# Performance work log

Hardware: AMD Instinct MI355X
Metric: run time of the kernel (lower is better)

The kernel has to match this reference:

```python
import jax, jax.numpy as jnp
import numpy as np

N_CH = 8      # n_channel (complex symbols)
L = 3         # channel taps
R = 0.5       # code rate k/n = 4/8
EBNO_DB = 7.0
EPS = 1e-5    # BatchNorm eps
NOISE_SCALE = float(1.0 / np.sqrt(2.0 * R * (10.0 ** (EBNO_DB / 10.0))))


def conv1d(x, w, b, stride=1):
    # x: [B, Cin, W], w: [Cout, Cin, K]
    y = jax.lax.conv_general_dilated(x, w, (stride,), 'VALID',
                                     dimension_numbers=('NCH', 'OIH', 'NCH'))
    return y + b[None, :, None]


def setup_inputs() -> dict:
    key = jax.random.key(0)
    ks = jax.random.split(key, 24)
    B = 262144
    s = 0.1  # weight scale for numerical stability
    inp = {
        'x': jax.random.normal(ks[0], (B, 16), jnp.float32),
        'noise': jax.random.normal(ks[1], (B, 16), jnp.float32),
        'fading': jax.random.normal(ks[2], (B, L, 2), jnp.float32) / np.sqrt(2.0),
        'ew1': jax.random.normal(ks[3], (16, 16), jnp.float32) * s,
        'eb1': jnp.zeros((16,), jnp.float32),
        'ew2': jax.random.normal(ks[4], (16, 16), jnp.float32) * s,
        'eb2': jnp.zeros((16,), jnp.float32),
        'bng': jnp.ones((16,), jnp.float32),
        'bnb': jnp.zeros((16,), jnp.float32),
        'pc1w': jax.random.normal(ks[5], (16, 1, 4), jnp.float32) * s,
        'pc1b': jnp.zeros((16,), jnp.float32),
        'pc2w': jax.random.normal(ks[6], (16, 16, 2), jnp.float32) * s,
        'pc2b': jnp.zeros((16,), jnp.float32),
        'pc3w': jax.random.normal(ks[7], (16, 16, 2), jnp.float32) * s,
        'pc3b': jnp.zeros((16,), jnp.float32),
        'pc4w': jax.random.normal(ks[8], (16, 16, 1), jnp.float32) * s,
        'pc4b': jnp.zeros((16,), jnp.float32),
        'pc5w': jax.random.normal(ks[9], (16, 16, 3), jnp.float32) * s,
        'pc5b': jnp.zeros((16,), jnp.float32),
        'plw': jax.random.normal(ks[10], (16, 16), jnp.float32) * s,
        'plb': jnp.ones((16,), jnp.float32),  # keep h estimate away from 0 (complex division)
        'dc1w': jax.random.normal(ks[11], (8, 1, 1), jnp.float32) * s,
        'dc1b': jnp.zeros((8,), jnp.float32),
        'dc2w': jax.random.normal(ks[12], (8, 8, 2), jnp.float32) * s,
        'dc2b': jnp.zeros((8,), jnp.float32),
        'dc3w': jax.random.normal(ks[13], (8, 8, 1), jnp.float32) * s,
        'dc3b': jnp.zeros((8,), jnp.float32),
        'dc4w': jax.random.normal(ks[14], (8, 8, 1), jnp.float32) * s,
        'dc4b': jnp.zeros((8,), jnp.float32),
        'dl1w': jax.random.normal(ks[15], (16, 64), jnp.float32) * s,
        'dl1b': jnp.zeros((16,), jnp.float32),
        'dl2w': jax.random.normal(ks[16], (16, 16), jnp.float32) * s,
        'dl2b': jnp.zeros((16,), jnp.float32),
        'dl3w': jax.random.normal(ks[17], (16, 16), jnp.float32) * s,
        'dl3b': jnp.zeros((16,), jnp.float32),
    }
    return inp


def reference(x, noise, fading, ew1, eb1, ew2, eb2, bng, bnb,
              pc1w, pc1b, pc2w, pc2b, pc3w, pc3b, pc4w, pc4b, pc5w, pc5b,
              plw, plb, dc1w, dc1b, dc2w, dc2b, dc3w, dc3b, dc4w, dc4b,
              dl1w, dl1b, dl2w, dl2b, dl3w, dl3b):
    B = x.shape[0]
    # ---- encoder: Linear -> ELU -> Linear -> BatchNorm1d (batch stats) ----
    h1 = jax.nn.elu(x @ ew1.T + eb1)
    z = h1 @ ew2.T + eb2
    mu = z.mean(0)
    var = ((z - mu) ** 2).mean(0)
    z = (z - mu) / jnp.sqrt(var + EPS) * bng + bnb
    # ---- rayleigh channel: complex FIR over L taps (vectorized) ----
    zc = z.reshape(B, N_CH, 2)
    c = jax.lax.complex(zc[..., 0], zc[..., 1])            # [B, 8] complex
    hf = jax.lax.complex(fading[..., 0], fading[..., 1])   # [B, 3] complex
    padded = jnp.pad(c, ((0, 0), (2, 2)))                  # [B, 12]
    idx = jnp.arange(N_CH + L - 1)[:, None] + jnp.arange(L)[None, :]  # [10, 3]
    win = padded[:, idx]                                   # [B, 10, 3]
    out = jnp.einsum('bij,bj->bi', win, hf[:, ::-1])[:, :N_CH]
    creal = jnp.stack([out.real, out.imag], -1).reshape(B, 2 * N_CH) + noise * NOISE_SCALE
    # ---- parameter estimation (conv stack) ----
    p = creal[:, None, :]                                  # [B, 1, 16]
    p = jax.nn.relu(conv1d(p, pc1w, pc1b, 1))              # [B,16,13]
    p = jax.nn.relu(conv1d(p, pc2w, pc2b, 1))              # [B,16,12]
    p = jax.nn.relu(conv1d(p, pc3w, pc3b, 4))              # [B,16,3]
    p = jax.nn.relu(conv1d(p, pc4w, pc4b, 1))              # [B,16,3]
    p = jax.nn.relu(conv1d(p, pc5w, pc5b, 1))              # [B,16,1]
    hhat = p.reshape(B, -1) @ plw.T + plb                  # [B,16]
    # ---- transform: complex equalization c / h ----
    cc2 = creal.reshape(B, N_CH, 2)
    hh2 = hhat.reshape(B, N_CH, 2)
    cc = jax.lax.complex(cc2[..., 0], cc2[..., 1])
    hh = jax.lax.complex(hh2[..., 0], hh2[..., 1])
    t = cc / hh
    treal = jnp.stack([t.real, t.imag], -1).reshape(B, 2 * N_CH)
    # ---- decoder (conv stack + MLP; dropout omitted / eval mode) ----
    d = treal[:, None, :]
    d = jax.nn.relu(conv1d(d, dc1w, dc1b, 1))              # [B,8,16]
    d = jax.nn.relu(conv1d(d, dc2w, dc2b, 2))              # [B,8,8]
    d = jax.nn.relu(conv1d(d, dc3w, dc3b, 1))
    d = jax.nn.relu(conv1d(d, dc4w, dc4b, 1))
    d = d.reshape(B, -1)                                   # [B,64]
    d = jax.nn.relu(d @ dl1w.T + dl1b)
    d = jax.nn.elu(d @ dl2w.T + dl2b)
    return d @ dl3w.T + dl3b
```

## Files before the change

kernel.cpp:

```cpp
#include <hip/hip_runtime.h>
#include <math.h>

#define NSCALE 0.44668359215096315f

typedef float v2f __attribute__((ext_vector_type(2)));

__device__ __forceinline__ v2f fma2(v2f a, v2f b, v2f c) { return __builtin_elementwise_fma(a, b, c); }
__device__ __forceinline__ float eluf(float v)  { return v > 0.0f ? v : __expf(v) - 1.0f; }
__device__ __forceinline__ float reluf(float v) { return fmaxf(v, 0.0f); }

__device__ __forceinline__ float dot16p(const float* __restrict__ w, const v2f p[8], float b) {
    const v2f* w2 = reinterpret_cast<const v2f*>(w);
    v2f a = {b, 0.0f};
#pragma unroll
    for (int q = 0; q < 8; ++q) a = fma2(w2[q], p[q], a);
    return a.x + a.y;
}
__device__ __forceinline__ float dot32p(const float* __restrict__ w, const v2f p[16], float b) {
    const v2f* w2 = reinterpret_cast<const v2f*>(w);
    v2f a = {b, 0.0f};
#pragma unroll
    for (int q = 0; q < 16; ++q) a = fma2(w2[q], p[q], a);
    return a.x + a.y;
}
__device__ __forceinline__ float dot8p(const float* __restrict__ w, const v2f p[4], float b) {
    const v2f* w2 = reinterpret_cast<const v2f*>(w);
    v2f a = {b, 0.0f};
#pragma unroll
    for (int q = 0; q < 4; ++q) a = fma2(w2[q], p[q], a);
    return a.x + a.y;
}

__global__ __launch_bounds__(256) void kW(const float* __restrict__ pc2w,
                                          const float* __restrict__ pc5w,
                                          const float* __restrict__ dl1w,
                                          float* __restrict__ pc2s,
                                          float* __restrict__ pc5s,
                                          float* __restrict__ dl1s)
{
    int tid = threadIdx.x;
    for (int j = tid; j < 512; j += 256) {
        int o = j >> 5, r = j & 31, ci = r >> 1, tap = r & 1;
        pc2s[tap*256 + o*16 + ci] = pc2w[j];
    }
    for (int j = tid; j < 768; j += 256) {
        int o = j / 48, r = j - o*48, ci = r / 3, g = r - ci*3;
        pc5s[g*256 + o*16 + ci] = pc5w[j];
    }
    for (int j = tid; j < 1024; j += 256) {
        int o = j >> 6, r = j & 63, c = r >> 3, t = r & 7;
        dl1s[t*128 + o*8 + c] = dl1w[j];
    }
}

__global__ __launch_bounds__(256) void kA(const float* __restrict__ x,
                                          const float* __restrict__ ew1, const float* __restrict__ eb1,
                                          const float* __restrict__ ew2, const float* __restrict__ eb2,
                                          float* __restrict__ partials, float* __restrict__ zout, int B)
{
    __shared__ float wsum[4][32];
    int tid = threadIdx.x;
    int i = blockIdx.x * 256 + tid;
    bool valid = i < B;
    v2f x2[8];
    if (valid) {
        const float4* xp = reinterpret_cast<const float4*>(x + (size_t)i * 16);
#pragma unroll
        for (int q = 0; q < 4; ++q) {
            float4 v = xp[q];
            x2[2*q+0] = {v.x, v.y};
            x2[2*q+1] = {v.z, v.w};
        }
    } else {
#pragma unroll
        for (int q = 0; q < 8; ++q) x2[q] = {0.0f, 0.0f};
    }

    v2f h1p[8];
#pragma unroll
    for (int j = 0; j < 8; ++j) {
        float r0 = eluf(dot16p(ew1 + (2*j+0)*16, x2, eb1[2*j+0]));
        float r1 = eluf(dot16p(ew1 + (2*j+1)*16, x2, eb1[2*j+1]));
        h1p[j] = {r0, r1};
    }
    float z[16];
#pragma unroll
    for (int o = 0; o < 16; ++o) {
        float a = dot16p(ew2 + o*16, h1p, eb2[o]);
        z[o] = valid ? a : 0.0f;
    }

    if (valid) {
        float4* zp = reinterpret_cast<float4*>(zout + (size_t)i * 16);
        zp[0] = make_float4(z[0],  z[1],  z[2],  z[3]);
        zp[1] = make_float4(z[4],  z[5],  z[6],  z[7]);
        zp[2] = make_float4(z[8],  z[9],  z[10], z[11]);
        zp[3] = make_float4(z[12], z[13], z[14], z[15]);
    }

    int lane = tid & 63, wave = tid >> 6;
#pragma unroll
    for (int c = 0; c < 16; ++c) {
        float s = z[c];
        float q = z[c] * z[c];
#pragma unroll
        for (int m = 1; m < 64; m <<= 1) { s += __shfl_xor(s, m); q += __shfl_xor(q, m); }
        if (lane == 0) { wsum[wave][c] = s; wsum[wave][16 + c] = q; }
    }
    __syncthreads();
    if (tid < 32) {
        float t = wsum[0][tid] + wsum[1][tid] + wsum[2][tid] + wsum[3][tid];
        partials[(size_t)blockIdx.x * 32 + tid] = t;
    }
}

__global__ __launch_bounds__(256) void kB(const float* __restrict__ partials, int nblk, int B,
                                          const float* __restrict__ bng, const float* __restrict__ bnb,
                                          float* __restrict__ bnp)
{
    int tid = threadIdx.x;
    int q = tid >> 3, k = tid & 7;
    int chunk = (nblk + 7) / 8;
    int j0 = k * chunk;
    int j1 = j0 + chunk; if (j1 > nblk) j1 = nblk;
    double s = 0.0;
    for (int j = j0; j < j1; ++j) s += (double)partials[(size_t)j * 32 + q];
    s += __shfl_xor(s, 4);
    s += __shfl_xor(s, 2);
    s += __shfl_xor(s, 1);
    __shared__ double tot[32];
    if (k == 0) tot[q] = s;
    __syncthreads();
    if (tid < 16) {
        double mu  = tot[tid] / (double)B;
        double var = tot[16 + tid] / (double)B - mu * mu;
        double a = (double)bng[tid] / sqrt(var + 1e-5);
        double b = (double)bnb[tid] - mu * a;
        bnp[tid]      = (float)a;
        bnp[16 + tid] = (float)b;
    }
}

__global__ __launch_bounds__(256) void k23(float* __restrict__ crt,
    const float* __restrict__ fading, const float* __restrict__ noise,
    const float* __restrict__ bnp,
    const float* __restrict__ pc1w, const float* __restrict__ pc1b,
    const float* __restrict__ pc2s, const float* __restrict__ pc2b,
    const float* __restrict__ pc3w, const float* __restrict__ pc3b,
    const float* __restrict__ pc4w, const float* __restrict__ pc4b,
    const float* __restrict__ pc5s, const float* __restrict__ pc5b,
    const float* __restrict__ plw,  const float* __restrict__ plb,
    int B)
{
    int i = blockIdx.x * 256 + threadIdx.x;
    if (i >= B) return;

    {
        float zn[16];
        const float4* zp = reinterpret_cast<const float4*>(crt + (size_t)i * 16);
#pragma unroll
        for (int q = 0; q < 4; ++q) {
            float4 v = zp[q];
            zn[4*q+0] = fmaf(v.x, bnp[4*q+0], bnp[16 + 4*q+0]);
            zn[4*q+1] = fmaf(v.y, bnp[4*q+1], bnp[16 + 4*q+1]);
            zn[4*q+2] = fmaf(v.z, bnp[4*q+2], bnp[16 + 4*q+2]);
            zn[4*q+3] = fmaf(v.w, bnp[4*q+3], bnp[16 + 4*q+3]);
        }
        float f[6];
        const float2* fp = reinterpret_cast<const float2*>(fading + (size_t)i * 6);
#pragma unroll
        for (int q = 0; q < 3; ++q) { float2 v = fp[q]; f[2*q] = v.x; f[2*q+1] = v.y; }
        float cr[16];
#pragma unroll
        for (int n = 0; n < 8; ++n) {
            float re = f[0]*zn[2*n]   - f[1]*zn[2*n+1];
            float im = f[0]*zn[2*n+1] + f[1]*zn[2*n];
            if (n >= 1) { re += f[2]*zn[2*n-2] - f[3]*zn[2*n-1];
                          im += f[2]*zn[2*n-1] + f[3]*zn[2*n-2]; }
            if (n >= 2) { re += f[4]*zn[2*n-4] - f[5]*zn[2*n-3];
                          im += f[4]*zn[2*n-3] + f[5]*zn[2*n-4]; }
            cr[2*n] = re; cr[2*n+1] = im;
        }
        const float4* np_ = reinterpret_cast<const float4*>(noise + (size_t)i * 16);
#pragma unroll
        for (int q = 0; q < 4; ++q) {
            float4 v = np_[q];
            cr[4*q+0] = fmaf(v.x, NSCALE, cr[4*q+0]);
            cr[4*q+1] = fmaf(v.y, NSCALE, cr[4*q+1]);
            cr[4*q+2] = fmaf(v.z, NSCALE, cr[4*q+2]);
            cr[4*q+3] = fmaf(v.w, NSCALE, cr[4*q+3]);
        }
        float4* op = reinterpret_cast<float4*>(crt + (size_t)i * 16);
        op[0] = make_float4(cr[0],  cr[1],  cr[2],  cr[3]);
        op[1] = make_float4(cr[4],  cr[5],  cr[6],  cr[7]);
        op[2] = make_float4(cr[8],  cr[9],  cr[10], cr[11]);
        op[3] = make_float4(cr[12], cr[13], cr[14], cr[15]);
    }

    v2f p5acc[16];
#pragma unroll
    for (int o = 0; o < 16; ++o) p5acc[o] = {pc5b[o], 0.0f};

#pragma unroll 1
    for (int g = 0; g < 3; ++g) {
        float crg[8];
        {
            const float4* cp = reinterpret_cast<const float4*>(crt + (size_t)i * 16 + 4 * g);
            float4 v0 = cp[0], v1 = cp[1];
            crg[0]=v0.x; crg[1]=v0.y; crg[2]=v0.z; crg[3]=v0.w;
            crg[4]=v1.x; crg[5]=v1.y; crg[6]=v1.z; crg[7]=v1.w;
        }
        v2f p1p[3][8];
#pragma unroll
        for (int c2 = 0; c2 < 3; ++c2) {
#pragma unroll
            for (int j = 0; j < 8; ++j) {
                float4 w0 = *reinterpret_cast<const float4*>(pc1w + (2*j+0)*4);
                float4 w1 = *reinterpret_cast<const float4*>(pc1w + (2*j+1)*4);
                float a0 = pc1b[2*j+0], a1 = pc1b[2*j+1];
                a0 = fmaf(w0.x, crg[c2+0], a0); a0 = fmaf(w0.y, crg[c2+1], a0);
                a0 = fmaf(w0.z, crg[c2+2], a0); a0 = fmaf(w0.w, crg[c2+3], a0);
                a1 = fmaf(w1.x, crg[c2+0], a1); a1 = fmaf(w1.y, crg[c2+1], a1);
                a1 = fmaf(w1.z, crg[c2+2], a1); a1 = fmaf(w1.w, crg[c2+3], a1);
                p1p[c2][j] = {reluf(a0), reluf(a1)};
            }
        }
        v2f p2pair[16];
#pragma unroll
        for (int o = 0; o < 16; ++o) {
            const v2f* w0 = reinterpret_cast<const v2f*>(pc2s + o*16);
            const v2f* w1 = reinterpret_cast<const v2f*>(pc2s + 256 + o*16);
            v2f a0 = {pc2b[o], 0.0f}, a1 = {pc2b[o], 0.0f};
#pragma unroll
            for (int q = 0; q < 8; ++q) {
                v2f v0 = w0[q], v1 = w1[q];
                a0 = fma2(v0, p1p[0][q], a0);
                a0 = fma2(v1, p1p[1][q], a0);
                a1 = fma2(v0, p1p[1][q], a1);
                a1 = fma2(v1, p1p[2][q], a1);
            }
            p2pair[o] = {reluf(a0.x + a0.y), reluf(a1.x + a1.y)};
        }
        v2f p3p[8];
#pragma unroll
        for (int j = 0; j < 8; ++j) {
            float r0 = reluf(dot32p(pc3w + (2*j+0)*32, p2pair, pc3b[2*j+0]));
            float r1 = reluf(dot32p(pc3w + (2*j+1)*32, p2pair, pc3b[2*j+1]));
            p3p[j] = {r0, r1};
        }
        v2f p4p[8];
#pragma unroll
        for (int j = 0; j < 8; ++j) {
            float r0 = reluf(dot16p(pc4w + (2*j+0)*16, p3p, pc4b[2*j+0]));
            float r1 = reluf(dot16p(pc4w + (2*j+1)*16, p3p, pc4b[2*j+1]));
            p4p[j] = {r0, r1};
        }
#pragma unroll
        for (int o = 0; o < 16; ++o) {
            const v2f* w = reinterpret_cast<const v2f*>(pc5s + g*256 + o*16);
            v2f a = p5acc[o];
#pragma unroll
            for (int q = 0; q < 8; ++q) a = fma2(w[q], p4p[q], a);
            p5acc[o] = a;
        }
    }

    v2f p5p[8];
#pragma unroll
    for (int j = 0; j < 8; ++j) {
        float r0 = reluf(p5acc[2*j+0].x + p5acc[2*j+0].y);
        float r1 = reluf(p5acc[2*j+1].x + p5acc[2*j+1].y);
        p5p[j] = {r0, r1};
    }
    float hh[16];
#pragma unroll
    for (int o = 0; o < 16; ++o) hh[o] = dot16p(plw + o*16, p5p, plb[o]);

    float cr[16];
    {
        const float4* cp = reinterpret_cast<const float4*>(crt + (size_t)i * 16);
#pragma unroll
        for (int q = 0; q < 4; ++q) {
            float4 v = cp[q];
            cr[4*q+0] = v.x; cr[4*q+1] = v.y; cr[4*q+2] = v.z; cr[4*q+3] = v.w;
        }
    }
    float tr[16];
#pragma unroll
    for (int n = 0; n < 8; ++n) {
        float a = cr[2*n], b = cr[2*n+1];
        float c = hh[2*n], d = hh[2*n+1];
        float inv = 1.0f / (c*c + d*d);
        tr[2*n]   = (a*c + b*d) * inv;
        tr[2*n+1] = (b*c - a*d) * inv;
    }
    float4* op = reinterpret_cast<float4*>(crt + (size_t)i * 16);
    op[0] = make_float4(tr[0],  tr[1],  tr[2],  tr[3]);
    op[1] = make_float4(tr[4],  tr[5],  tr[6],  tr[7]);
    op[2] = make_float4(tr[8],  tr[9],  tr[10], tr[11]);
    op[3] = make_float4(tr[12], tr[13], tr[14], tr[15]);
}

__global__ __launch_bounds__(256) void k4(const float* __restrict__ trt,
    const float* __restrict__ dc1w, const float* __restrict__ dc1b,
    const float* __restrict__ dc2w, const float* __restrict__ dc2b,
    const float* __restrict__ dc3w, const float* __restrict__ dc3b,
    const float* __restrict__ dc4w, const float* __restrict__ dc4b,
    const float* __restrict__ dl1s, const float* __restrict__ dl1b,
    const float* __restrict__ dl2w, const float* __restrict__ dl2b,
    const float* __restrict__ dl3w, const float* __restrict__ dl3b,
    float* __restrict__ out, int B)
{
    int i = blockIdx.x * 256 + threadIdx.x;
    if (i >= B) return;

    v2f y2[16];
#pragma unroll
    for (int o = 0; o < 16; ++o) y2[o] = {dl1b[o], 0.0f};

#pragma unroll 1
    for (int t = 0; t < 8; ++t) {
        float2 tv = *reinterpret_cast<const float2*>(trt + (size_t)i * 16 + 2 * t);
        v2f d1p[8];
#pragma unroll
        for (int c = 0; c < 8; ++c) {
            float w = dc1w[c], b = dc1b[c];
            d1p[c] = {reluf(fmaf(w, tv.x, b)), reluf(fmaf(w, tv.y, b))};
        }
        v2f d2p[4];
#pragma unroll
        for (int j = 0; j < 4; ++j) {
            float r0 = reluf(dot16p(dc2w + (2*j+0)*16, d1p, dc2b[2*j+0]));
            float r1 = reluf(dot16p(dc2w + (2*j+1)*16, d1p, dc2b[2*j+1]));
            d2p[j] = {r0, r1};
        }
        v2f d3p[4];
#pragma unroll
        for (int j = 0; j < 4; ++j) {
            float r0 = reluf(dot8p(dc3w + (2*j+0)*8, d2p, dc3b[2*j+0]));
            float r1 = reluf(dot8p(dc3w + (2*j+1)*8, d2p, dc3b[2*j+1]));
            d3p[j] = {r0, r1};
        }
        v2f d4p[4];
#pragma unroll
        for (int j = 0; j < 4; ++j) {
            float r0 = reluf(dot8p(dc4w + (2*j+0)*8, d3p, dc4b[2*j+0]));
            float r1 = reluf(dot8p(dc4w + (2*j+1)*8, d3p, dc4b[2*j+1]));
            d4p[j] = {r0, r1};
        }
#pragma unroll
        for (int o = 0; o < 16; ++o) {
            const v2f* w = reinterpret_cast<const v2f*>(dl1s + t*128 + o*8);
            v2f a = y2[o];
#pragma unroll
            for (int q = 0; q < 4; ++q) a = fma2(w[q], d4p[q], a);
            y2[o] = a;
        }
    }

    v2f yp[8];
#pragma unroll
    for (int j = 0; j < 8; ++j) {
        float r0 = reluf(y2[2*j+0].x + y2[2*j+0].y);
        float r1 = reluf(y2[2*j+1].x + y2[2*j+1].y);
        yp[j] = {r0, r1};
    }
    v2f h2p[8];
#pragma unroll
    for (int j = 0; j < 8; ++j) {
        float r0 = eluf(dot16p(dl2w + (2*j+0)*16, yp, dl2b[2*j+0]));
        float r1 = eluf(dot16p(dl2w + (2*j+1)*16, yp, dl2b[2*j+1]));
        h2p[j] = {r0, r1};
    }
    float o16[16];
#pragma unroll
    for (int o = 0; o < 16; ++o) o16[o] = dot16p(dl3w + o*16, h2p, dl3b[o]);

    float4* op = reinterpret_cast<float4*>(out + (size_t)i * 16);
    op[0] = make_float4(o16[0],  o16[1],  o16[2],  o16[3]);
    op[1] = make_float4(o16[4],  o16[5],  o16[6],  o16[7]);
    op[2] = make_float4(o16[8],  o16[9],  o16[10], o16[11]);
    op[3] = make_float4(o16[12], o16[13], o16[14], o16[15]);
}

extern "C" void kernel_launch(void* const* d_in, const int* in_sizes, int n_in,
                              void* d_out, int out_size, void* d_ws, size_t ws_size,
                              hipStream_t stream)
{
    const float* x      = (const float*)d_in[0];
    const float* noise  = (const float*)d_in[1];
    const float* fading = (const float*)d_in[2];
    const float* ew1  = (const float*)d_in[3];
    const float* eb1  = (const float*)d_in[4];
    const float* ew2  = (const float*)d_in[5];
    const float* eb2  = (const float*)d_in[6];
    const float* bng  = (const float*)d_in[7];
    const float* bnb  = (const float*)d_in[8];
    const float* pc1w = (const float*)d_in[9];
    const float* pc1b = (const float*)d_in[10];
    const float* pc2w = (const float*)d_in[11];
    const float* pc2b = (const float*)d_in[12];
    const float* pc3w = (const float*)d_in[13];
    const float* pc3b = (const float*)d_in[14];
    const float* pc4w = (const float*)d_in[15];
    const float* pc4b = (const float*)d_in[16];
    const float* pc5w = (const float*)d_in[17];
    const float* pc5b = (const float*)d_in[18];
    const float* plw  = (const float*)d_in[19];
    const float* plb  = (const float*)d_in[20];
    const float* dc1w = (const float*)d_in[21];
    const float* dc1b = (const float*)d_in[22];
    const float* dc2w = (const float*)d_in[23];
    const float* dc2b = (const float*)d_in[24];
    const float* dc3w = (const float*)d_in[25];
    const float* dc3b = (const float*)d_in[26];
    const float* dc4w = (const float*)d_in[27];
    const float* dc4b = (const float*)d_in[28];
    const float* dl1w = (const float*)d_in[29];
    const float* dl1b = (const float*)d_in[30];
    const float* dl2w = (const float*)d_in[31];
    const float* dl2b = (const float*)d_in[32];
    const float* dl3w = (const float*)d_in[33];
    const float* dl3b = (const float*)d_in[34];

    int B = in_sizes[0] / 16;
    int nblk = (B + 255) / 256;

    float* partials = (float*)d_ws;
    float* bnp  = partials + (size_t)nblk * 32;
    float* pc2s = bnp + 32;
    float* pc5s = pc2s + 512;
    float* dl1s = pc5s + 768;
    float* crt  = dl1s + 1024;

    kW<<<1, 256, 0, stream>>>(pc2w, pc5w, dl1w, pc2s, pc5s, dl1s);
    kA<<<nblk, 256, 0, stream>>>(x, ew1, eb1, ew2, eb2, partials, crt, B);
    kB<<<1, 256, 0, stream>>>(partials, nblk, B, bng, bnb, bnp);
    k23<<<nblk, 256, 0, stream>>>(crt, fading, noise, bnp,
                                  pc1w, pc1b, pc2s, pc2b, pc3w, pc3b, pc4w, pc4b, pc5s, pc5b,
                                  plw, plb, B);
    k4<<<nblk, 256, 0, stream>>>(crt,
                                 dc1w, dc1b, dc2w, dc2b, dc3w, dc3b, dc4w, dc4b,
                                 dl1s, dl1b, dl2w, dl2b, dl3w, dl3b,
                                 (float*)d_out, B);
}
```

Measured before the change: 227.8 us.

## Fuse weight prep into encoder kernel and merge pilot and decoder kernels

The weight-transpose kernel becomes an extra block of the encoder kernel, and the channel/pilot-estimation kernel is fused with the decoder kernel. This removes two launches and one global round-trip of the equalized signal between kernels. The pc1 conv weights are also re-laid out so each step can use packed v2f FMAs, and the dc1 layer is vectorized the same way. The fused kernel is larger and may use more registers, which could lower occupancy. It still writes the equalized values to global memory and reads them back within the same thread.

New measurement: 226.2 us. No clear change (-0.7%).

```diff
diff --git a/kernel.cpp b/kernel.cpp
--- a/kernel.cpp
+++ b/kernel.cpp
@@ -6,6 +6,8 @@
 typedef float v2f __attribute__((ext_vector_type(2)));
 
 __device__ __forceinline__ v2f fma2(v2f a, v2f b, v2f c) { return __builtin_elementwise_fma(a, b, c); }
+__device__ __forceinline__ v2f s2(float w) { v2f r = {w, w}; return r; }
+__device__ __forceinline__ v2f max0(v2f v) { v2f z = {0.0f, 0.0f}; return __builtin_elementwise_max(v, z); }
 __device__ __forceinline__ float eluf(float v)  { return v > 0.0f ? v : __expf(v) - 1.0f; }
 __device__ __forceinline__ float reluf(float v) { return fmaxf(v, 0.0f); }
 
@@ -31,35 +33,37 @@
     return a.x + a.y;
 }
 
-__global__ __launch_bounds__(256) void kW(const float* __restrict__ pc2w,
-                                          const float* __restrict__ pc5w,
-                                          const float* __restrict__ dl1w,
-                                          float* __restrict__ pc2s,
-                                          float* __restrict__ pc5s,
-                                          float* __restrict__ dl1s)
+__global__ __launch_bounds__(256) void kAW(const float* __restrict__ x,
+                                           const float* __restrict__ ew1, const float* __restrict__ eb1,
+                                           const float* __restrict__ ew2, const float* __restrict__ eb2,
+                                           float* __restrict__ partials, float* __restrict__ zout, int B,
+                                           const float* __restrict__ pc1w, const float* __restrict__ pc2w,
+                                           const float* __restrict__ pc5w, const float* __restrict__ dl1w,
+                                           float* __restrict__ pc1i, float* __restrict__ pc2s,
+                                           float* __restrict__ pc5s, float* __restrict__ dl1s)
 {
     int tid = threadIdx.x;
-    for (int j = tid; j < 512; j += 256) {
-        int o = j >> 5, r = j & 31, ci = r >> 1, tap = r & 1;
-        pc2s[tap*256 + o*16 + ci] = pc2w[j];
-    }
-    for (int j = tid; j < 768; j += 256) {
-        int o = j / 48, r = j - o*48, ci = r / 3, g = r - ci*3;
-        pc5s[g*256 + o*16 + ci] = pc5w[j];
-    }
-    for (int j = tid; j < 1024; j += 256) {
-        int o = j >> 6, r = j & 63, c = r >> 3, t = r & 7;
-        dl1s[t*128 + o*8 + c] = dl1w[j];
-    }
-}
-
-__global__ __launch_bounds__(256) void kA(const float* __restrict__ x,
-                                          const float* __restrict__ ew1, const float* __restrict__ eb1,
-                                          const float* __restrict__ ew2, const float* __restrict__ eb2,
-                                          float* __restrict__ partials, float* __restrict__ zout, int B)
-{
+    if (blockIdx.x == gridDim.x - 1) {
+        for (int n = tid; n < 64; n += 256) {
+            int j = n >> 3, k = (n >> 1) & 3, h = n & 1;
+            pc1i[n] = pc1w[(2*j + h)*4 + k];
+        }
+        for (int j = tid; j < 512; j += 256) {
+            int o = j >> 5, r = j & 31, ci = r >> 1, tap = r & 1;
+            pc2s[tap*256 + o*16 + ci] = pc2w[j];
+        }
+        for (int j = tid; j < 768; j += 256) {
+            int o = j / 48, r = j - o*48, ci = r / 3, g = r - ci*3;
+            pc5s[g*256 + o*16 + ci] = pc5w[j];
+        }
+        for (int j = tid; j < 1024; j += 256) {
+            int o = j >> 6, r = j & 63, c = r >> 3, t = r & 7;
+            dl1s[t*128 + o*8 + c] = dl1w[j];
+        }
+        return;
+    }
+
     __shared__ float wsum[4][32];
-    int tid = threadIdx.x;
     int i = blockIdx.x * 256 + tid;
     bool valid = i < B;
     v2f x2[8];
@@ -141,167 +145,15 @@
     }
 }
 
-__global__ __launch_bounds__(256) void k23(float* __restrict__ crt,
+__global__ __launch_bounds__(256) void kF(float* __restrict__ crt,
     const float* __restrict__ fading, const float* __restrict__ noise,
     const float* __restrict__ bnp,
-    const float* __restrict__ pc1w, const float* __restrict__ pc1b,
+    const float* __restrict__ pc1i, const float* __restrict__ pc1b,
     const float* __restrict__ pc2s, const float* __restrict__ pc2b,
     const float* __restrict__ pc3w, const float* __restrict__ pc3b,
     const float* __restrict__ pc4w, const float* __restrict__ pc4b,
     const float* __restrict__ pc5s, const float* __restrict__ pc5b,
     const float* __restrict__ plw,  const float* __restrict__ plb,
-    int B)
-{
-    int i = blockIdx.x * 256 + threadIdx.x;
-    if (i >= B) return;
-
-    {
-        float zn[16];
-        const float4* zp = reinterpret_cast<const float4*>(crt + (size_t)i * 16);
-#pragma unroll
-        for (int q = 0; q < 4; ++q) {
-            float4 v = zp[q];
-            zn[4*q+0] = fmaf(v.x, bnp[4*q+0], bnp[16 + 4*q+0]);
-            zn[4*q+1] = fmaf(v.y, bnp[4*q+1], bnp[16 + 4*q+1]);
-            zn[4*q+2] = fmaf(v.z, bnp[4*q+2], bnp[16 + 4*q+2]);
-            zn[4*q+3] = fmaf(v.w, bnp[4*q+3], bnp[16 + 4*q+3]);
-        }
-        float f[6];
-        const float2* fp = reinterpret_cast<const float2*>(fading + (size_t)i * 6);
-#pragma unroll
-        for (int q = 0; q < 3; ++q) { float2 v = fp[q]; f[2*q] = v.x; f[2*q+1] = v.y; }
-        float cr[16];
-#pragma unroll
-        for (int n = 0; n < 8; ++n) {
-            float re = f[0]*zn[2*n]   - f[1]*zn[2*n+1];
-            float im = f[0]*zn[2*n+1] + f[1]*zn[2*n];
-            if (n >= 1) { re += f[2]*zn[2*n-2] - f[3]*zn[2*n-1];
-                          im += f[2]*zn[2*n-1] + f[3]*zn[2*n-2]; }
-            if (n >= 2) { re += f[4]*zn[2*n-4] - f[5]*zn[2*n-3];
-                          im += f[4]*zn[2*n-3] + f[5]*zn[2*n-4]; }
-            cr[2*n] = re; cr[2*n+1] = im;
-        }
-        const float4* np_ = reinterpret_cast<const float4*>(noise + (size_t)i * 16);
-#pragma unroll
-        for (int q = 0; q < 4; ++q) {
-            float4 v = np_[q];
-            cr[4*q+0] = fmaf(v.x, NSCALE, cr[4*q+0]);
-            cr[4*q+1] = fmaf(v.y, NSCALE, cr[4*q+1]);
-            cr[4*q+2] = fmaf(v.z, NSCALE, cr[4*q+2]);
-            cr[4*q+3] = fmaf(v.w, NSCALE, cr[4*q+3]);
-        }
-        float4* op = reinterpret_cast<float4*>(crt + (size_t)i * 16);
-        op[0] = make_float4(cr[0],  cr[1],  cr[2],  cr[3]);
-        op[1] = make_float4(cr[4],  cr[5],  cr[6],  cr[7]);
-        op[2] = make_float4(cr[8],  cr[9],  cr[10], cr[11]);
-        op[3] = make_float4(cr[12], cr[13], cr[14], cr[15]);
-    }
-
-    v2f p5acc[16];
-#pragma unroll
-    for (int o = 0; o < 16; ++o) p5acc[o] = {pc5b[o], 0.0f};
-
-#pragma unroll 1
-    for (int g = 0; g < 3; ++g) {
-        float crg[8];
-        {
-            const float4* cp = reinterpret_cast<const float4*>(crt + (size_t)i * 16 + 4 * g);
-            float4 v0 = cp[0], v1 = cp[1];
-            crg[0]=v0.x; crg[1]=v0.y; crg[2]=v0.z; crg[3]=v0.w;
-            crg[4]=v1.x; crg[5]=v1.y; crg[6]=v1.z; crg[7]=v1.w;
-        }
-        v2f p1p[3][8];
-#pragma unroll
-        for (int c2 = 0; c2 < 3; ++c2) {
-#pragma unroll
-            for (int j = 0; j < 8; ++j) {
-                float4 w0 = *reinterpret_cast<const float4*>(pc1w + (2*j+0)*4);
-                float4 w1 = *reinterpret_cast<const float4*>(pc1w + (2*j+1)*4);
-                float a0 = pc1b[2*j+0], a1 = pc1b[2*j+1];
-                a0 = fmaf(w0.x, crg[c2+0], a0); a0 = fmaf(w0.y, crg[c2+1], a0);
-                a0 = fmaf(w0.z, crg[c2+2], a0); a0 = fmaf(w0.w, crg[c2+3], a0);
-                a1 = fmaf(w1.x, crg[c2+0], a1); a1 = fmaf(w1.y, crg[c2+1], a1);
-                a1 = fmaf(w1.z, crg[c2+2], a1); a1 = fmaf(w1.w, crg[c2+3], a1);
-                p1p[c2][j] = {reluf(a0), reluf(a1)};
-            }
-        }
-        v2f p2pair[16];
-#pragma unroll
-        for (int o = 0; o < 16; ++o) {
-            const v2f* w0 = reinterpret_cast<const v2f*>(pc2s + o*16);
-            const v2f* w1 = reinterpret_cast<const v2f*>(pc2s + 256 + o*16);
-            v2f a0 = {pc2b[o], 0.0f}, a1 = {pc2b[o], 0.0f};
-#pragma unroll
-            for (int q = 0; q < 8; ++q) {
-                v2f v0 = w0[q], v1 = w1[q];
-                a0 = fma2(v0, p1p[0][q], a0);
-                a0 = fma2(v1, p1p[1][q], a0);
-                a1 = fma2(v0, p1p[1][q], a1);
-                a1 = fma2(v1, p1p[2][q], a1);
-            }
-            p2pair[o] = {reluf(a0.x + a0.y), reluf(a1.x + a1.y)};
-        }
-        v2f p3p[8];
-#pragma unroll
-        for (int j = 0; j < 8; ++j) {
-            float r0 = reluf(dot32p(pc3w + (2*j+0)*32, p2pair, pc3b[2*j+0]));
-            float r1 = reluf(dot32p(pc3w + (2*j+1)*32, p2pair, pc3b[2*j+1]));
-            p3p[j] = {r0, r1};
-        }
-        v2f p4p[8];
-#pragma unroll
-        for (int j = 0; j < 8; ++j) {
-            float r0 = reluf(dot16p(pc4w + (2*j+0)*16, p3p, pc4b[2*j+0]));
-            float r1 = reluf(dot16p(pc4w + (2*j+1)*16, p3p, pc4b[2*j+1]));
-            p4p[j] = {r0, r1};
-        }
-#pragma unroll
-        for (int o = 0; o < 16; ++o) {
-            const v2f* w = reinterpret_cast<const v2f*>(pc5s + g*256 + o*16);
-            v2f a = p5acc[o];
-#pragma unroll
-            for (int q = 0; q < 8; ++q) a = fma2(w[q], p4p[q], a);
-            p5acc[o] = a;
-        }
-    }
-
-    v2f p5p[8];
-#pragma unroll
-    for (int j = 0; j < 8; ++j) {
-        float r0 = reluf(p5acc[2*j+0].x + p5acc[2*j+0].y);
-        float r1 = reluf(p5acc[2*j+1].x + p5acc[2*j+1].y);
-        p5p[j] = {r0, r1};
-    }
-    float hh[16];
-#pragma unroll
-    for (int o = 0; o < 16; ++o) hh[o] = dot16p(plw + o*16, p5p, plb[o]);
-
-    float cr[16];
-    {
-        const float4* cp = reinterpret_cast<const float4*>(crt + (size_t)i * 16);
-#pragma unroll
-        for (int q = 0; q < 4; ++q) {
-            float4 v = cp[q];
-            cr[4*q+0] = v.x; cr[4*q+1] = v.y; cr[4*q+2] = v.z; cr[4*q+3] = v.w;
-        }
-    }
-    float tr[16];
-#pragma unroll
-    for (int n = 0; n < 8; ++n) {
-        float a = cr[2*n], b = cr[2*n+1];
-        float c = hh[2*n], d = hh[2*n+1];
-        float inv = 1.0f / (c*c + d*d);
-        tr[2*n]   = (a*c + b*d) * inv;
-        tr[2*n+1] = (b*c - a*d) * inv;
-    }
-    float4* op = reinterpret_cast<float4*>(crt + (size_t)i * 16);
-    op[0] = make_float4(tr[0],  tr[1],  tr[2],  tr[3]);
-    op[1] = make_float4(tr[4],  tr[5],  tr[6],  tr[7]);
-    op[2] = make_float4(tr[8],  tr[9],  tr[10], tr[11]);
-    op[3] = make_float4(tr[12], tr[13], tr[14], tr[15]);
-}
-
-__global__ __launch_bounds__(256) void k4(const float* __restrict__ trt,
     const float* __restrict__ dc1w, const float* __restrict__ dc1b,
     const float* __restrict__ dc2w, const float* __restrict__ dc2b,
     const float* __restrict__ dc3w, const float* __restrict__ dc3b,
@@ -314,18 +166,162 @@
     int i = blockIdx.x * 256 + threadIdx.x;
     if (i >= B) return;
 
+    {
+        float zn[16];
+        const float4* zp = reinterpret_cast<const float4*>(crt + (size_t)i * 16);
+#pragma unroll
+        for (int q = 0; q < 4; ++q) {
+            float4 v = zp[q];
+            zn[4*q+0] = fmaf(v.x, bnp[4*q+0], bnp[16 + 4*q+0]);
+            zn[4*q+1] = fmaf(v.y, bnp[4*q+1], bnp[16 + 4*q+1]);
+            zn[4*q+2] = fmaf(v.z, bnp[4*q+2], bnp[16 + 4*q+2]);
+            zn[4*q+3] = fmaf(v.w, bnp[4*q+3], bnp[16 + 4*q+3]);
+        }
+        float f[6];
+        const float2* fp = reinterpret_cast<const float2*>(fading + (size_t)i * 6);
+#pragma unroll
+        for (int q = 0; q < 3; ++q) { float2 v = fp[q]; f[2*q] = v.x; f[2*q+1] = v.y; }
+        float cr[16];
+#pragma unroll
+        for (int n = 0; n < 8; ++n) {
+            float re = f[0]*zn[2*n]   - f[1]*zn[2*n+1];
+            float im = f[0]*zn[2*n+1] + f[1]*zn[2*n];
+            if (n >= 1) { re += f[2]*zn[2*n-2] - f[3]*zn[2*n-1];
+                          im += f[2]*zn[2*n-1] + f[3]*zn[2*n-2]; }
+            if (n >= 2) { re += f[4]*zn[2*n-4] - f[5]*zn[2*n-3];
+                          im += f[4]*zn[2*n-3] + f[5]*zn[2*n-4]; }
+            cr[2*n] = re; cr[2*n+1] = im;
+        }
+        const float4* np_ = reinterpret_cast<const float4*>(noise + (size_t)i * 16);
+#pragma unroll
+        for (int q = 0; q < 4; ++q) {
+            float4 v = np_[q];
+            cr[4*q+0] = fmaf(v.x, NSCALE, cr[4*q+0]);
+            cr[4*q+1] = fmaf(v.y, NSCALE, cr[4*q+1]);
+            cr[4*q+2] = fmaf(v.z, NSCALE, cr[4*q+2]);
+            cr[4*q+3] = fmaf(v.w, NSCALE, cr[4*q+3]);
+        }
+        float4* op = reinterpret_cast<float4*>(crt + (size_t)i * 16);
+        op[0] = make_float4(cr[0],  cr[1],  cr[2],  cr[3]);
+        op[1] = make_float4(cr[4],  cr[5],  cr[6],  cr[7]);
+        op[2] = make_float4(cr[8],  cr[9],  cr[10], cr[11]);
+        op[3] = make_float4(cr[12], cr[13], cr[14], cr[15]);
+    }
+
+    v2f p5acc[16];
+#pragma unroll
+    for (int o = 0; o < 16; ++o) p5acc[o] = {pc5b[o], 0.0f};
+
+#pragma unroll 1
+    for (int g = 0; g < 3; ++g) {
+        float crg[8];
+        {
+            const float4* cp = reinterpret_cast<const float4*>(crt + (size_t)i * 16 + 4 * g);
+            float4 v0 = cp[0], v1 = cp[1];
+            crg[0]=v0.x; crg[1]=v0.y; crg[2]=v0.z; crg[3]=v0.w;
+            crg[4]=v1.x; crg[5]=v1.y; crg[6]=v1.z; crg[7]=v1.w;
+        }
+        v2f p1p[3][8];
+#pragma unroll
+        for (int c2 = 0; c2 < 3; ++c2) {
+#pragma unroll
+            for (int j = 0; j < 8; ++j) {
+                const v2f* wi = reinterpret_cast<const v2f*>(pc1i + j*8);
+                v2f a = *reinterpret_cast<const v2f*>(pc1b + 2*j);
+                a = fma2(wi[0], s2(crg[c2+0]), a);
+                a = fma2(wi[1], s2(crg[c2+1]), a);
+                a = fma2(wi[2], s2(crg[c2+2]), a);
+                a = fma2(wi[3], s2(crg[c2+3]), a);
+                p1p[c2][j] = max0(a);
+            }
+        }
+        v2f p2pair[16];
+#pragma unroll
+        for (int o = 0; o < 16; ++o) {
+            const v2f* w0 = reinterpret_cast<const v2f*>(pc2s + o*16);
+            const v2f* w1 = reinterpret_cast<const v2f*>(pc2s + 256 + o*16);
+            v2f a0 = {pc2b[o], 0.0f}, a1 = {pc2b[o], 0.0f};
+#pragma unroll
+            for (int q = 0; q < 8; ++q) {
+                v2f v0 = w0[q], v1 = w1[q];
+                a0 = fma2(v0, p1p[0][q], a0);
+                a0 = fma2(v1, p1p[1][q], a0);
+                a1 = fma2(v0, p1p[1][q], a1);
+                a1 = fma2(v1, p1p[2][q], a1);
+            }
+            p2pair[o] = {reluf(a0.x + a0.y), reluf(a1.x + a1.y)};
+        }
+        v2f p3p[8];
+#pragma unroll
+        for (int j = 0; j < 8; ++j) {
+            float r0 = reluf(dot32p(pc3w + (2*j+0)*32, p2pair, pc3b[2*j+0]));
+            float r1 = reluf(dot32p(pc3w + (2*j+1)*32, p2pair, pc3b[2*j+1]));
+            p3p[j] = {r0, r1};
+        }
+        v2f p4p[8];
+#pragma unroll
+        for (int j = 0; j < 8; ++j) {
+            float r0 = reluf(dot16p(pc4w + (2*j+0)*16, p3p, pc4b[2*j+0]));
+            float r1 = reluf(dot16p(pc4w + (2*j+1)*16, p3p, pc4b[2*j+1]));
+            p4p[j] = {r0, r1};
+        }
+#pragma unroll
+        for (int o = 0; o < 16; ++o) {
+            const v2f* w = reinterpret_cast<const v2f*>(pc5s + g*256 + o*16);
+            v2f a = p5acc[o];
+#pragma unroll
+            for (int q = 0; q < 8; ++q) a = fma2(w[q], p4p[q], a);
+            p5acc[o] = a;
+        }
+    }
+
+    v2f p5p[8];
+#pragma unroll
+    for (int j = 0; j < 8; ++j) {
+        float r0 = reluf(p5acc[2*j+0].x + p5acc[2*j+0].y);
+        float r1 = reluf(p5acc[2*j+1].x + p5acc[2*j+1].y);
+        p5p[j] = {r0, r1};
+    }
+    float hh[16];
+#pragma unroll
+    for (int o = 0; o < 16; ++o) hh[o] = dot16p(plw + o*16, p5p, plb[o]);
+
+    {
+        float cr[16];
+        const float4* cp = reinterpret_cast<const float4*>(crt + (size_t)i * 16);
+#pragma unroll
+        for (int q = 0; q < 4; ++q) {
+            float4 v = cp[q];
+            cr[4*q+0] = v.x; cr[4*q+1] = v.y; cr[4*q+2] = v.z; cr[4*q+3] = v.w;
+        }
+        float tr[16];
+#pragma unroll
+        for (int n = 0; n < 8; ++n) {
+            float a = cr[2*n], b = cr[2*n+1];
+            float c = hh[2*n], d = hh[2*n+1];
+            float inv = 1.0f / (c*c + d*d);
+            tr[2*n]   = (a*c + b*d) * inv;
+            tr[2*n+1] = (b*c - a*d) * inv;
+        }
+        float4* op = reinterpret_cast<float4*>(crt + (size_t)i * 16);
+        op[0] = make_float4(tr[0],  tr[1],  tr[2],  tr[3]);
+        op[1] = make_float4(tr[4],  tr[5],  tr[6],  tr[7]);
+        op[2] = make_float4(tr[8],  tr[9],  tr[10], tr[11]);
+        op[3] = make_float4(tr[12], tr[13], tr[14], tr[15]);
+    }
+
     v2f y2[16];
 #pragma unroll
     for (int o = 0; o < 16; ++o) y2[o] = {dl1b[o], 0.0f};
 
 #pragma unroll 1
     for (int t = 0; t < 8; ++t) {
-        float2 tv = *reinterpret_cast<const float2*>(trt + (size_t)i * 16 + 2 * t);
+        float2 tv = *reinterpret_cast<const float2*>(crt + (size_t)i * 16 + 2 * t);
+        v2f tv2 = {tv.x, tv.y};
         v2f d1p[8];
 #pragma unroll
         for (int c = 0; c < 8; ++c) {
-            float w = dc1w[c], b = dc1b[c];
-            d1p[c] = {reluf(fmaf(w, tv.x, b)), reluf(fmaf(w, tv.y, b))};
+            d1p[c] = max0(fma2(s2(dc1w[c]), tv2, s2(dc1b[c])));
         }
         v2f d2p[4];
 #pragma unroll
@@ -431,15 +427,16 @@
     float* pc2s = bnp + 32;
     float* pc5s = pc2s + 512;
     float* dl1s = pc5s + 768;
-    float* crt  = dl1s + 1024;
-
-    kW<<<1, 256, 0, stream>>>(pc2w, pc5w, dl1w, pc2s, pc5s, dl1s);
-    kA<<<nblk, 256, 0, stream>>>(x, ew1, eb1, ew2, eb2, partials, crt, B);
+    float* pc1i = dl1s + 1024;
+    float* crt  = pc1i + 128;
+
+    kAW<<<nblk + 1, 256, 0, stream>>>(x, ew1, eb1, ew2, eb2, partials, crt, B,
+                                      pc1w, pc2w, pc5w, dl1w,
+                                      pc1i, pc2s, pc5s, dl1s);
     kB<<<1, 256, 0, stream>>>(partials, nblk, B, bng, bnb, bnp);
-    k23<<<nblk, 256, 0, stream>>>(crt, fading, noise, bnp,
-                                  pc1w, pc1b, pc2s, pc2b, pc3w, pc3b, pc4w, pc4b, pc5s, pc5b,
-                                  plw, plb, B);
-    k4<<<nblk, 256, 0, stream>>>(crt,
+    kF<<<nblk, 256, 0, stream>>>(crt, fading, noise, bnp,
+                                 pc1i, pc1b, pc2s, pc2b, pc3w, pc3b, pc4w, pc4b, pc5s, pc5b,
+                                 plw, plb,
                                  dc1w, dc1b, dc2w, dc2b, dc3w, dc3b, dc4w, dc4b,
                                  dl1s, dl1b, dl2w, dl2b, dl3w, dl3b,
                                  (float*)d_out, B);
```
